# Kernel tuning notes

Measured on AMD Instinct MI355X. Metric: run time of the kernel, lower is better.

The kernel has to match this reference:

```python
import jax, jax.numpy as jnp
import numpy as np

D_MODEL = 1024
NUM_HEADS = 16
DEPTH = D_MODEL // NUM_HEADS


def setup_inputs() -> dict:
    key = jax.random.key(0)
    ks = jax.random.split(key, 11)
    B, S = 4, 2048
    scale = 1.0 / np.sqrt(D_MODEL)
    inp = {
        "query": jax.random.normal(ks[0], (B, S, D_MODEL), jnp.float32),
        "key": jax.random.normal(ks[1], (B, S, D_MODEL), jnp.float32),
        "value": jax.random.normal(ks[2], (B, S, D_MODEL), jnp.float32),
        # Linear params (torch nn.Linear: y = x @ W.T + b); store W as [out, in]
        "wq_w": jax.random.normal(ks[3], (D_MODEL, D_MODEL), jnp.float32) * scale,
        "wq_b": jnp.zeros((D_MODEL,), jnp.float32),
        "wk_w": jax.random.normal(ks[4], (D_MODEL, D_MODEL), jnp.float32) * scale,
        "wk_b": jnp.zeros((D_MODEL,), jnp.float32),
        "wv_w": jax.random.normal(ks[5], (D_MODEL, D_MODEL), jnp.float32) * scale,
        "wv_b": jnp.zeros((D_MODEL,), jnp.float32),
        "dense_w": jax.random.normal(ks[6], (D_MODEL, D_MODEL), jnp.float32) * scale,
        "dense_b": jnp.zeros((D_MODEL,), jnp.float32),
    }
    return inp


def _split_heads(x, B):
    # [B, S, D] -> [B, H, S, depth]
    return x.reshape(B, -1, NUM_HEADS, DEPTH).transpose(0, 2, 1, 3)


def reference(query, key, value, wq_w, wq_b, wk_w, wk_b, wv_w, wv_b, dense_w, dense_b):
    B = query.shape[0]
    q = _split_heads(query @ wq_w.T + wq_b, B)   # [B,H,Sq,depth]
    k = _split_heads(key @ wk_w.T + wk_b, B)     # [B,H,Sk,depth]
    v = _split_heads(value @ wv_w.T + wv_b, B)   # [B,H,Sk,depth]
    scores = jnp.einsum("bhqd,bhkd->bhqk", q, k) / jnp.sqrt(jnp.float32(DEPTH)).astype(q.dtype)
    attn = jax.nn.softmax(scores, axis=-1)
    out = jnp.einsum("bhqk,bhkd->bhqd", attn, v)  # [B,H,Sq,depth]
    out = out.transpose(0, 2, 1, 3).reshape(B, -1, D_MODEL)
    return out @ dense_w.T + dense_b
```

## Files before the change

kernel.cpp:

```cpp
#include <hip/hip_runtime.h>
#include <hip/hip_bf16.h>
#include <stdint.h>


#define SEQ    2048
#define DEPTH  64
#define HEADS  16
#define NMODEL 1024
#define MROWS  8192

typedef __bf16 bf16x8 __attribute__((ext_vector_type(8)));
typedef float  f32x4  __attribute__((ext_vector_type(4)));

__device__ __forceinline__ unsigned short f32_bf16(float f) {
    union { float f; unsigned int u; } c; c.f = f;
    unsigned int u = c.u + 0x7FFFu + ((c.u >> 16) & 1u);
    return (unsigned short)(u >> 16);
}

__device__ __forceinline__ void gload16(const unsigned short* g, unsigned short* l) {
    __builtin_amdgcn_global_load_lds(
        (const __attribute__((address_space(1))) unsigned int*)g,
        (__attribute__((address_space(3))) unsigned int*)l, 16, 0, 0);
}

__global__ __launch_bounds__(256) void cvt3_kernel(
    const float* __restrict__ a, const float* __restrict__ b, const float* __restrict__ c,
    unsigned short* __restrict__ oa, unsigned short* __restrict__ ob,
    unsigned short* __restrict__ oc, int n4)
{
    const float* in; unsigned short* out;
    if (blockIdx.y == 0) { in = a; out = oa; }
    else if (blockIdx.y == 1) { in = b; out = ob; }
    else { in = c; out = oc; }
    int i = blockIdx.x * 256 + threadIdx.x;
    if (i < n4) {
        float4 f = ((const float4*)in)[i];
        ushort4 o;
        o.x = f32_bf16(f.x); o.y = f32_bf16(f.y);
        o.z = f32_bf16(f.z); o.w = f32_bf16(f.w);
        ((ushort4*)out)[i] = o;
    }
}

__global__ __launch_bounds__(256) void cvt4_kernel(
    const float* __restrict__ a, const float* __restrict__ b,
    const float* __restrict__ c, const float* __restrict__ d,
    unsigned short* __restrict__ oa, unsigned short* __restrict__ ob,
    unsigned short* __restrict__ oc, unsigned short* __restrict__ od, int n4)
{
    const float* in; unsigned short* out;
    if (blockIdx.y == 0) { in = a; out = oa; }
    else if (blockIdx.y == 1) { in = b; out = ob; }
    else if (blockIdx.y == 2) { in = c; out = oc; }
    else { in = d; out = od; }
    int i = blockIdx.x * 256 + threadIdx.x;
    if (i < n4) {
        float4 f = ((const float4*)in)[i];
        ushort4 o;
        o.x = f32_bf16(f.x); o.y = f32_bf16(f.y);
        o.z = f32_bf16(f.z); o.w = f32_bf16(f.w);
        ((ushort4*)out)[i] = o;
    }
}

__device__ __forceinline__ void gemm128_core(
    const unsigned short* __restrict__ A, const unsigned short* __restrict__ W,
    const float* __restrict__ bias, void* __restrict__ outp,
    int mode, float scale, int m0, int n0,
    unsigned short* Alds, unsigned short* Blds)
{
    const int tid  = threadIdx.x;
    const int wave = tid >> 6, lane = tid & 63;
    const int l15  = lane & 15, quad = lane >> 4;
    const int wm   = wave & 1,  wn   = wave >> 1;
    const int swz  = l15 & 7;
    const int K    = 1024;

    f32x4 acc[4][4] = {};

    const int lrow = lane >> 3;
    const int fcol = ((lane & 7) ^ lrow) << 3;
    const unsigned short* Ab[4];
    const unsigned short* Bb[4];
    #pragma unroll
    for (int c = 0; c < 4; ++c) {
        const int seg = 4 * wave + c;
        Ab[c] = A + (size_t)(m0 + seg * 8 + lrow) * K + fcol;
        Bb[c] = W + (size_t)(n0 + seg * 8 + lrow) * K + fcol;
    }

    for (int k0 = 0; k0 < K; k0 += 64) {
        #pragma unroll
        for (int c = 0; c < 4; ++c) {
            gload16(Ab[c] + k0, &Alds[(4 * wave + c) * 512]);
            gload16(Bb[c] + k0, &Blds[(4 * wave + c) * 512]);
        }
        __syncthreads();

        #pragma unroll
        for (int kc = 0; kc < 2; ++kc) {
            bf16x8 a[4], b[4];
            const int pg = (((kc * 4 + quad) ^ swz) << 3);
            #pragma unroll
            for (int i = 0; i < 4; ++i)
                a[i] = *(const bf16x8*)&Alds[(wm * 64 + i * 16 + l15) * 64 + pg];
            #pragma unroll
            for (int j = 0; j < 4; ++j)
                b[j] = *(const bf16x8*)&Blds[(wn * 64 + j * 16 + l15) * 64 + pg];
            #pragma unroll
            for (int i = 0; i < 4; ++i)
                #pragma unroll
                for (int j = 0; j < 4; ++j)
                    acc[i][j] = __builtin_amdgcn_mfma_f32_16x16x32_bf16(a[i], b[j], acc[i][j], 0, 0, 0);
        }
        __syncthreads();
    }

    #pragma unroll
    for (int i = 0; i < 4; ++i) {
        #pragma unroll
        for (int j = 0; j < 4; ++j) {
            const int col = n0 + wn * 64 + j * 16 + l15;
            const int row_b = m0 + wm * 64 + i * 16 + quad * 4;
            if (mode == 2) {
                #pragma unroll
                for (int r = 0; r < 4; ++r) {
                    const int row = row_b + r;
                    ((unsigned short*)outp)[(size_t)row * MROWS + col] =
                        f32_bf16(acc[i][j][r] + bias[row]);
                }
            } else if (mode == 0) {
                const float bv = bias[col];
                #pragma unroll
                for (int r = 0; r < 4; ++r)
                    ((float*)outp)[(size_t)(row_b + r) * NMODEL + col] = acc[i][j][r] + bv;
            } else {
                const float bv = bias[col];
                const int h_ = col >> 6, d_ = col & 63;
                #pragma unroll
                for (int r = 0; r < 4; ++r) {
                    const int row = row_b + r;
                    const int b_ = row >> 11, s_ = row & 2047;
                    ((unsigned short*)outp)[(((size_t)(b_ * HEADS + h_) * SEQ + s_) << 6) + d_] =
                        f32_bf16((acc[i][j][r] + bv) * scale);
                }
            }
        }
    }
}

__global__ __launch_bounds__(256, 3) void gemm_qkv(
    const unsigned short* __restrict__ qb,  const unsigned short* __restrict__ wqb,
    const float* __restrict__ bq, unsigned short* __restrict__ Qp,
    const unsigned short* __restrict__ kb,  const unsigned short* __restrict__ wkb,
    const float* __restrict__ bk, unsigned short* __restrict__ Kpj,
    const unsigned short* __restrict__ wvb, const unsigned short* __restrict__ vb,
    const float* __restrict__ bv, unsigned short* __restrict__ Vtg,
    float qscale)
{
    __shared__ unsigned short Alds[128 * 64];
    __shared__ unsigned short Blds[128 * 64];
    const int bid = blockIdx.x, z = blockIdx.y;
    if (z == 0) {
        gemm128_core(qb, wqb, bq, Qp, 1, qscale, (bid >> 3) * 128, (bid & 7) * 128, Alds, Blds);
    } else if (z == 1) {
        gemm128_core(kb, wkb, bk, Kpj, 1, 1.0f, (bid >> 3) * 128, (bid & 7) * 128, Alds, Blds);
    } else {
        gemm128_core(wvb, vb, bv, Vtg, 2, 1.0f, (bid & 7) * 128, (bid >> 3) * 128, Alds, Blds);
    }
}

__global__ __launch_bounds__(256, 3) void gemm_dense(
    const unsigned short* __restrict__ A, const unsigned short* __restrict__ W,
    const float* __restrict__ bias, float* __restrict__ out)
{
    __shared__ unsigned short Alds[128 * 64];
    __shared__ unsigned short Blds[128 * 64];
    const int bid = blockIdx.x;
    gemm128_core(A, W, bias, out, 0, 1.0f, (bid >> 3) * 128, (bid & 7) * 128, Alds, Blds);
}

__global__ __launch_bounds__(256, 4) void attn_fwd(
    const unsigned short* __restrict__ Qp,
    const unsigned short* __restrict__ Kp,
    const unsigned short* __restrict__ Vtg,
    unsigned short* __restrict__ Op)
{
    __shared__ unsigned short Klds[64 * 64];
    __shared__ unsigned short Vlds[64 * 64];
    __shared__ unsigned short Pt[4 * 32 * 64];
    const int tid  = threadIdx.x;
    const int wave = tid >> 6, lane = tid & 63;
    const int l15  = lane & 15, quad = lane >> 4;
    const int swz  = l15 & 7;
    const int bh   = blockIdx.y;
    const int b_   = bh >> 4, h_ = bh & 15;
    const int q0   = blockIdx.x * 128;

    const unsigned short* Qb = Qp + (size_t)bh * SEQ * DEPTH;
    const unsigned short* Kb = Kp + (size_t)bh * SEQ * DEPTH;
    const unsigned short* Vb = Vtg + (size_t)h_ * DEPTH * MROWS + (size_t)b_ * SEQ;

    const int srow = (wave << 3) + (lane >> 3);
    const int scg  = (lane & 7) ^ ((lane >> 3) & 7);
    unsigned short* KldsW = &Klds[wave * 512];
    unsigned short* VldsW = &Vlds[wave * 512];
    unsigned short* PtW   = &Pt[wave * 2048];

    bf16x8 qf[2][2];
    #pragma unroll
    for (int i = 0; i < 2; ++i)
        #pragma unroll
        for (int kc = 0; kc < 2; ++kc)
            qf[i][kc] = *(const bf16x8*)(Qb + (size_t)(q0 + wave * 32 + i * 16 + l15) * DEPTH
                                         + kc * 32 + quad * 8);

    f32x4 Ot[2][4] = {};
    float lsum[2] = {0.f, 0.f};

    for (int kt = 0; kt < SEQ / 64; ++kt) {
        const int kb0 = kt * 64;
        gload16(Kb + (size_t)(kb0 + srow) * DEPTH + scg * 8,      KldsW);
        gload16(Kb + (size_t)(kb0 + srow + 32) * DEPTH + scg * 8, KldsW + 2048);
        gload16(Vb + (size_t)srow * MROWS + kb0 + scg * 8,        VldsW);
        gload16(Vb + (size_t)(srow + 32) * MROWS + kb0 + scg * 8, VldsW + 2048);
        __syncthreads();

        f32x4 St[2][4];
        #pragma unroll
        for (int i = 0; i < 2; ++i)
            #pragma unroll
            for (int jj = 0; jj < 4; ++jj)
                St[i][jj] = f32x4{};
        #pragma unroll
        for (int jj = 0; jj < 4; ++jj) {
            bf16x8 k0 = *(const bf16x8*)&Klds[(jj * 16 + l15) * 64 + (((quad    ) ^ swz) << 3)];
            bf16x8 k1 = *(const bf16x8*)&Klds[(jj * 16 + l15) * 64 + (((4 + quad) ^ swz) << 3)];
            #pragma unroll
            for (int i = 0; i < 2; ++i) {
                St[i][jj] = __builtin_amdgcn_mfma_f32_16x16x32_bf16(k0, qf[i][0], St[i][jj], 0, 0, 0);
                St[i][jj] = __builtin_amdgcn_mfma_f32_16x16x32_bf16(k1, qf[i][1], St[i][jj], 0, 0, 0);
            }
        }

        #pragma unroll
        for (int i = 0; i < 2; ++i) {
            #pragma unroll
            for (int jj = 0; jj < 4; ++jj) {
                float p0 = __builtin_amdgcn_exp2f(St[i][jj][0]);
                float p1 = __builtin_amdgcn_exp2f(St[i][jj][1]);
                float p2 = __builtin_amdgcn_exp2f(St[i][jj][2]);
                float p3 = __builtin_amdgcn_exp2f(St[i][jj][3]);
                lsum[i] += (p0 + p1) + (p2 + p3);
                __hip_bfloat162 pa = __float22bfloat162_rn(make_float2(p0, p1));
                __hip_bfloat162 pb = __float22bfloat162_rn(make_float2(p2, p3));
                uint2 pw = { *(unsigned int*)&pa, *(unsigned int*)&pb };
                *(uint2*)&PtW[(i * 16 + l15) * 64 +
                              (((2 * jj + (quad >> 1)) ^ swz) << 3) + (quad & 1) * 4] = pw;
            }
        }

        #pragma unroll
        for (int kc = 0; kc < 2; ++kc) {
            const int pg = (((kc * 4 + quad) ^ swz) << 3);
            bf16x8 vf[4];
            #pragma unroll
            for (int dd = 0; dd < 4; ++dd)
                vf[dd] = *(const bf16x8*)&Vlds[(dd * 16 + l15) * 64 + pg];
            #pragma unroll
            for (int i = 0; i < 2; ++i) {
                bf16x8 pf = *(const bf16x8*)&PtW[(i * 16 + l15) * 64 + pg];
                #pragma unroll
                for (int dd = 0; dd < 4; ++dd)
                    Ot[i][dd] = __builtin_amdgcn_mfma_f32_16x16x32_bf16(vf[dd], pf, Ot[i][dd], 0, 0, 0);
            }
        }
        __syncthreads();
    }

    #pragma unroll
    for (int i = 0; i < 2; ++i) {
        lsum[i] += __shfl_xor(lsum[i], 16, 64);
        lsum[i] += __shfl_xor(lsum[i], 32, 64);
    }

    #pragma unroll
    for (int i = 0; i < 2; ++i) {
        const float inv = 1.0f / lsum[i];
        const int row = b_ * SEQ + q0 + wave * 32 + i * 16 + l15;
        #pragma unroll
        for (int dd = 0; dd < 4; ++dd) {
            ushort4 ov;
            ov.x = f32_bf16(Ot[i][dd][0] * inv);
            ov.y = f32_bf16(Ot[i][dd][1] * inv);
            ov.z = f32_bf16(Ot[i][dd][2] * inv);
            ov.w = f32_bf16(Ot[i][dd][3] * inv);
            const int col = h_ * 64 + dd * 16 + quad * 4;
            *(ushort4*)&Op[(size_t)row * NMODEL + col] = ov;
        }
    }
}

extern "C" void kernel_launch(void* const* d_in, const int* in_sizes, int n_in,
                              void* d_out, int out_size, void* d_ws, size_t ws_size,
                              hipStream_t stream) {
    const float* q  = (const float*)d_in[0];
    const float* k  = (const float*)d_in[1];
    const float* v  = (const float*)d_in[2];
    const float* wq = (const float*)d_in[3];
    const float* bq = (const float*)d_in[4];
    const float* wk = (const float*)d_in[5];
    const float* bk = (const float*)d_in[6];
    const float* wv = (const float*)d_in[7];
    const float* bv = (const float*)d_in[8];
    const float* wd = (const float*)d_in[9];
    const float* bd = (const float*)d_in[10];

    char* ws = (char*)d_ws;
    size_t off = 0;
    auto alloc = [&](size_t bytes) { char* p = ws + off; off += bytes; return p; };
    const size_t ACT = (size_t)MROWS * NMODEL * 2;
    const size_t WGT = (size_t)NMODEL * NMODEL * 2;

    unsigned short* qb   = (unsigned short*)alloc(ACT);
    unsigned short* kb   = (unsigned short*)alloc(ACT);
    unsigned short* vb   = (unsigned short*)alloc(ACT);
    unsigned short* wqb  = (unsigned short*)alloc(WGT);
    unsigned short* wkb  = (unsigned short*)alloc(WGT);
    unsigned short* wvb  = (unsigned short*)alloc(WGT);
    unsigned short* wdb  = (unsigned short*)alloc(WGT);
    unsigned short* Qp   = (unsigned short*)alloc(ACT);
    unsigned short* Kpj  = (unsigned short*)alloc(ACT);
    unsigned short* Vtg  = (unsigned short*)alloc(ACT);
    unsigned short* attn = (unsigned short*)alloc(ACT);

    const int nAct4 = MROWS * NMODEL / 4;
    const int nWgt4 = NMODEL * NMODEL / 4;
    cvt3_kernel<<<dim3(nAct4 / 256, 3), 256, 0, stream>>>(q, k, v, qb, kb, vb, nAct4);
    cvt4_kernel<<<dim3(nWgt4 / 256, 4), 256, 0, stream>>>(wq, wk, wv, wd,
                                                          wqb, wkb, wvb, wdb, nWgt4);

    const float SC = 0.18033688011112042f;
    gemm_qkv<<<dim3(512, 3), 256, 0, stream>>>(qb, wqb, bq, Qp,
                                               kb, wkb, bk, Kpj,
                                               wvb, vb, bv, Vtg, SC);

    attn_fwd<<<dim3(SEQ / 128, 64), 256, 0, stream>>>(Qp, Kpj, Vtg, attn);

    gemm_dense<<<512, 256, 0, stream>>>(attn, wdb, bd, (float*)d_out);
}
```

Before: 349.5 us.

## Double-buffer K/V tiles and keep P in registers in attention kernel

```diff
diff --git a/kernel.cpp b/kernel.cpp
--- a/kernel.cpp
+++ b/kernel.cpp
@@ -10,6 +10,7 @@
 #define MROWS  8192
 
 typedef __bf16 bf16x8 __attribute__((ext_vector_type(8)));
+typedef __bf16 bf16x4 __attribute__((ext_vector_type(4)));
 typedef float  f32x4  __attribute__((ext_vector_type(4)));
 
 __device__ __forceinline__ unsigned short f32_bf16(float f) {
@@ -187,9 +188,8 @@
     const unsigned short* __restrict__ Vtg,
     unsigned short* __restrict__ Op)
 {
-    __shared__ unsigned short Klds[64 * 64];
-    __shared__ unsigned short Vlds[64 * 64];
-    __shared__ unsigned short Pt[4 * 32 * 64];
+    __shared__ unsigned short Klds[2 * 64 * 64];
+    __shared__ unsigned short Vlds[2 * 64 * 64];
     const int tid  = threadIdx.x;
     const int wave = tid >> 6, lane = tid & 63;
     const int l15  = lane & 15, quad = lane >> 4;
@@ -204,9 +204,11 @@
 
     const int srow = (wave << 3) + (lane >> 3);
     const int scg  = (lane & 7) ^ ((lane >> 3) & 7);
-    unsigned short* KldsW = &Klds[wave * 512];
-    unsigned short* VldsW = &Vlds[wave * 512];
-    unsigned short* PtW   = &Pt[wave * 2048];
+
+    const unsigned short* Kg0 = Kb + (size_t)srow * DEPTH + scg * 8;
+    const unsigned short* Kg1 = Kb + (size_t)(srow + 32) * DEPTH + scg * 8;
+    const unsigned short* Vg0 = Vb + (size_t)srow * MROWS + scg * 8;
+    const unsigned short* Vg1 = Vb + (size_t)(srow + 32) * MROWS + scg * 8;
 
     bf16x8 qf[2][2];
     #pragma unroll
@@ -216,78 +218,94 @@
             qf[i][kc] = *(const bf16x8*)(Qb + (size_t)(q0 + wave * 32 + i * 16 + l15) * DEPTH
                                          + kc * 32 + quad * 8);
 
+    union { bf16x8 v; unsigned short s[8]; } uo;
+    #pragma unroll
+    for (int j = 0; j < 8; ++j) uo.s[j] = 0x3F80;
+    const bf16x8 ones = uo.v;
+
     f32x4 Ot[2][4] = {};
-    float lsum[2] = {0.f, 0.f};
+    f32x4 lacc[2]  = {};
+
+    auto STAGE = [&](int buf, int kt) {
+        unsigned short* KW = &Klds[buf * 4096 + wave * 512];
+        unsigned short* VW = &Vlds[buf * 4096 + wave * 512];
+        gload16(Kg0 + (size_t)kt * 4096, KW);
+        gload16(Kg1 + (size_t)kt * 4096, KW + 2048);
+        gload16(Vg0 + kt * 64, VW);
+        gload16(Vg1 + kt * 64, VW + 2048);
+    };
+
+    STAGE(0, 0);
+    asm volatile("s_waitcnt vmcnt(0)" ::: "memory");
+    __builtin_amdgcn_s_barrier();
 
     for (int kt = 0; kt < SEQ / 64; ++kt) {
-        const int kb0 = kt * 64;
-        gload16(Kb + (size_t)(kb0 + srow) * DEPTH + scg * 8,      KldsW);
-        gload16(Kb + (size_t)(kb0 + srow + 32) * DEPTH + scg * 8, KldsW + 2048);
-        gload16(Vb + (size_t)srow * MROWS + kb0 + scg * 8,        VldsW);
-        gload16(Vb + (size_t)(srow + 32) * MROWS + kb0 + scg * 8, VldsW + 2048);
-        __syncthreads();
-
-        f32x4 St[2][4];
+        const int cur = kt & 1;
+        if (kt + 1 < SEQ / 64) STAGE(cur ^ 1, kt + 1);
+
+        const unsigned short* Kc = &Klds[cur * 4096];
+        const unsigned short* Vc = &Vlds[cur * 4096];
+
+        f32x4 St[2][4] = {};
+        #pragma unroll
+        for (int jj = 0; jj < 4; ++jj) {
+            bf16x8 k0 = *(const bf16x8*)&Kc[(jj * 16 + l15) * 64 + ((quad ^ swz) << 3)];
+            bf16x8 k1 = *(const bf16x8*)&Kc[(jj * 16 + l15) * 64 + (((4 + quad) ^ swz) << 3)];
+            St[0][jj] = __builtin_amdgcn_mfma_f32_16x16x32_bf16(k0, qf[0][0], St[0][jj], 0, 0, 0);
+            St[0][jj] = __builtin_amdgcn_mfma_f32_16x16x32_bf16(k1, qf[0][1], St[0][jj], 0, 0, 0);
+            St[1][jj] = __builtin_amdgcn_mfma_f32_16x16x32_bf16(k0, qf[1][0], St[1][jj], 0, 0, 0);
+            St[1][jj] = __builtin_amdgcn_mfma_f32_16x16x32_bf16(k1, qf[1][1], St[1][jj], 0, 0, 0);
+        }
+
         #pragma unroll
         for (int i = 0; i < 2; ++i)
             #pragma unroll
             for (int jj = 0; jj < 4; ++jj)
-                St[i][jj] = f32x4{};
-        #pragma unroll
-        for (int jj = 0; jj < 4; ++jj) {
-            bf16x8 k0 = *(const bf16x8*)&Klds[(jj * 16 + l15) * 64 + (((quad    ) ^ swz) << 3)];
-            bf16x8 k1 = *(const bf16x8*)&Klds[(jj * 16 + l15) * 64 + (((4 + quad) ^ swz) << 3)];
-            #pragma unroll
-            for (int i = 0; i < 2; ++i) {
-                St[i][jj] = __builtin_amdgcn_mfma_f32_16x16x32_bf16(k0, qf[i][0], St[i][jj], 0, 0, 0);
-                St[i][jj] = __builtin_amdgcn_mfma_f32_16x16x32_bf16(k1, qf[i][1], St[i][jj], 0, 0, 0);
+                #pragma unroll
+                for (int r = 0; r < 4; ++r)
+                    St[i][jj][r] = __builtin_amdgcn_exp2f(St[i][jj][r]);
+
+        bf16x8 pf[2][2];
+        #pragma unroll
+        for (int i = 0; i < 2; ++i)
+            #pragma unroll
+            for (int kc = 0; kc < 2; ++kc) {
+                union { bf16x8 v; __hip_bfloat162 h[4]; } up;
+                up.h[0] = __float22bfloat162_rn(make_float2(St[i][2 * kc][0],     St[i][2 * kc][1]));
+                up.h[1] = __float22bfloat162_rn(make_float2(St[i][2 * kc][2],     St[i][2 * kc][3]));
+                up.h[2] = __float22bfloat162_rn(make_float2(St[i][2 * kc + 1][0], St[i][2 * kc + 1][1]));
+                up.h[3] = __float22bfloat162_rn(make_float2(St[i][2 * kc + 1][2], St[i][2 * kc + 1][3]));
+                pf[i][kc] = up.v;
             }
-        }
-
-        #pragma unroll
-        for (int i = 0; i < 2; ++i) {
-            #pragma unroll
-            for (int jj = 0; jj < 4; ++jj) {
-                float p0 = __builtin_amdgcn_exp2f(St[i][jj][0]);
-                float p1 = __builtin_amdgcn_exp2f(St[i][jj][1]);
-                float p2 = __builtin_amdgcn_exp2f(St[i][jj][2]);
-                float p3 = __builtin_amdgcn_exp2f(St[i][jj][3]);
-                lsum[i] += (p0 + p1) + (p2 + p3);
-                __hip_bfloat162 pa = __float22bfloat162_rn(make_float2(p0, p1));
-                __hip_bfloat162 pb = __float22bfloat162_rn(make_float2(p2, p3));
-                uint2 pw = { *(unsigned int*)&pa, *(unsigned int*)&pb };
-                *(uint2*)&PtW[(i * 16 + l15) * 64 +
-                              (((2 * jj + (quad >> 1)) ^ swz) << 3) + (quad & 1) * 4] = pw;
+
+        lacc[0] = __builtin_amdgcn_mfma_f32_16x16x32_bf16(ones, pf[0][0], lacc[0], 0, 0, 0);
+        lacc[0] = __builtin_amdgcn_mfma_f32_16x16x32_bf16(ones, pf[0][1], lacc[0], 0, 0, 0);
+        lacc[1] = __builtin_amdgcn_mfma_f32_16x16x32_bf16(ones, pf[1][0], lacc[1], 0, 0, 0);
+        lacc[1] = __builtin_amdgcn_mfma_f32_16x16x32_bf16(ones, pf[1][1], lacc[1], 0, 0, 0);
+
+        #pragma unroll
+        for (int kc = 0; kc < 2; ++kc) {
+            const int glo = ((kc * 4 + (quad >> 1)) ^ swz);
+            const int ghi = ((kc * 4 + 2 + (quad >> 1)) ^ swz);
+            const int sub = (quad & 1) * 4;
+            #pragma unroll
+            for (int dd = 0; dd < 4; ++dd) {
+                const int row = (dd * 16 + l15) * 64;
+                union { bf16x8 v; bf16x4 h[2]; } uv;
+                uv.h[0] = *(const bf16x4*)&Vc[row + glo * 8 + sub];
+                uv.h[1] = *(const bf16x4*)&Vc[row + ghi * 8 + sub];
+                Ot[0][dd] = __builtin_amdgcn_mfma_f32_16x16x32_bf16(uv.v, pf[0][kc], Ot[0][dd], 0, 0, 0);
+                Ot[1][dd] = __builtin_amdgcn_mfma_f32_16x16x32_bf16(uv.v, pf[1][kc], Ot[1][dd], 0, 0, 0);
             }
         }
 
-        #pragma unroll
-        for (int kc = 0; kc < 2; ++kc) {
-            const int pg = (((kc * 4 + quad) ^ swz) << 3);
-            bf16x8 vf[4];
-            #pragma unroll
-            for (int dd = 0; dd < 4; ++dd)
-                vf[dd] = *(const bf16x8*)&Vlds[(dd * 16 + l15) * 64 + pg];
-            #pragma unroll
-            for (int i = 0; i < 2; ++i) {
-                bf16x8 pf = *(const bf16x8*)&PtW[(i * 16 + l15) * 64 + pg];
-                #pragma unroll
-                for (int dd = 0; dd < 4; ++dd)
-                    Ot[i][dd] = __builtin_amdgcn_mfma_f32_16x16x32_bf16(vf[dd], pf, Ot[i][dd], 0, 0, 0);
-            }
-        }
-        __syncthreads();
+        asm volatile("s_waitcnt vmcnt(0)" ::: "memory");
+        __builtin_amdgcn_s_barrier();
     }
 
     #pragma unroll
     for (int i = 0; i < 2; ++i) {
-        lsum[i] += __shfl_xor(lsum[i], 16, 64);
-        lsum[i] += __shfl_xor(lsum[i], 32, 64);
-    }
-
-    #pragma unroll
-    for (int i = 0; i < 2; ++i) {
-        const float inv = 1.0f / lsum[i];
+        const float inv = 1.0f / lacc[i][0];
         const int row = b_ * SEQ + q0 + wave * 32 + i * 16 + l15;
         #pragma unroll
         for (int dd = 0; dd < 4; ++dd) {
```

New measurement: 330.0 us. 1.06x faster.
